# Performance work log

Measured on AMD Instinct MI355X. Metric: run time of the kernel, lower is better.

The kernel has to match this reference:

```python
import jax, jax.numpy as jnp
import numpy as np

N_HP = 49152   # healpix nodes (12 * 4**6)
N_DST = 50000  # destination feature nodes
E = 400000     # edges per edge type (avg in-degree 8)
T_OUT = 4      # output_length
H = 64         # hidden_size
HID = 128      # attention hidden = 2*hidden_size


def setup_inputs() -> dict:
    key = jax.random.key(0)
    ks = jax.random.split(key, 9)
    s = 0.1
    return {
        "x": jax.random.normal(ks[0], (N_HP, T_OUT, 1, H), jnp.float32),
        "prev0": jax.random.normal(ks[1], (N_DST, 1), jnp.float32),
        "conv_W": s * jax.random.normal(ks[2], (T_OUT, H, H), jnp.float32),
        "conv_b": jnp.zeros((T_OUT, H), jnp.float32),
        "lin_W": s * jax.random.normal(ks[3], (1, H), jnp.float32),
        "lin_b": jnp.zeros((H,), jnp.float32),
        "att_W1": s * jax.random.normal(ks[4], (H, HID), jnp.float32),
        "att_b1": jnp.zeros((HID,), jnp.float32),
        "att_W2": s * jax.random.normal(ks[5], (HID, 1), jnp.float32),
        "att_b2": jnp.zeros((1,), jnp.float32),
        "dec_W": s * jax.random.normal(ks[6], (H, 1), jnp.float32),
        "dec_b": jnp.zeros((1,), jnp.float32),
        "src_idx": jax.random.randint(ks[7], (T_OUT, E), 0, N_HP),
        "dst_idx": jax.random.randint(ks[8], (T_OUT, E), 0, N_DST),
    }


def _graph_conv(src_feat, s_idx, d_idx, W, b):
    # dgl.nn.GraphConv with norm='both', bias, activation=LeakyReLU(0.01)
    ones = jnp.ones(s_idx.shape[0], src_feat.dtype)
    out_deg = jax.ops.segment_sum(ones, s_idx, num_segments=N_HP)
    in_deg = jax.ops.segment_sum(ones, d_idx, num_segments=N_DST)
    h = src_feat * jax.lax.rsqrt(jnp.clip(out_deg, 1.0))[:, None]   # D_src^{-1/2} X
    agg = jax.ops.segment_sum(h[s_idx], d_idx, num_segments=N_DST)  # gather [E,H] + scatter-add
    agg = agg * jax.lax.rsqrt(jnp.clip(in_deg, 1.0))[:, None]       # D_dst^{-1/2}
    return jax.nn.leaky_relu(agg @ W + b, negative_slope=0.01)


def reference(x, prev0, conv_W, conv_b, lin_W, lin_b, att_W1, att_b1,
              att_W2, att_b2, dec_W, dec_b, src_idx, dst_idx):
    prev = prev0  # node data at t = input_length - 1, shape [N_DST, 1]
    outs = []
    for t in range(T_OUT):  # sequential over horizon (prev feeds back)
        feat = x[:, t, 0]  # [N_HP, H]
        # HeteroGraphConv(aggregate='sum'): every edge type's GraphConv fires
        # on the same healpix src features; per-dst-node results are summed.
        space1 = jnp.zeros((N_DST, H), x.dtype)
        for tt in range(T_OUT):
            space1 = space1 + _graph_conv(feat, src_idx[tt], dst_idx[tt],
                                          conv_W[tt], conv_b[tt])
        space2 = prev @ lin_W + lin_b            # self.linears on prev step [N_DST, H]
        s = jnp.stack([space1, space2], 0)[None]  # [1, 2, N_DST, H]
        # AttentionReadout: soft attention over dim=1 (the 2 space branches)
        logits = jnp.tanh(s @ att_W1 + att_b1) @ att_W2 + att_b2  # [1,2,N,1]
        alpha = jax.nn.softmax(logits, axis=1)
        states = (alpha * s).sum(axis=1)          # [1, N_DST, H]
        out = states @ dec_W + dec_b              # [1, N_DST, 1] (horizon=1)
        prev = out[0]                             # stored back into node data
        outs.append(prev)
    return jnp.stack(outs, axis=0)  # [T_OUT, N_DST, 1]
```

## Files before the change

kernel.cpp:

```cpp
#include <hip/hip_runtime.h>

#define N_HP 49152
#define N_DST 50000
#define NE 400000
#define H 64
#define HID 128
#define DEG_CAP 64

typedef __attribute__((ext_vector_type(8))) short bf16x8;
typedef __attribute__((ext_vector_type(4))) float f32x4;

__device__ __forceinline__ ushort f2bf(float f) {
    uint u = __float_as_uint(f);
    u += 0x7fffu + ((u >> 16) & 1);
    return (ushort)(u >> 16);
}

#define BF2LO(u) __uint_as_float((u) << 16)
#define BF2HI(u) __uint_as_float((u) & 0xffff0000u)

#define XC_N (N_HP * 64)
__global__ __launch_bounds__(256) void k_prep(const float* __restrict__ x,
                                              uint* __restrict__ xb,
                                              const int* __restrict__ src_idx,
                                              const int* __restrict__ dst_idx,
                                              int* __restrict__ cnt_src,
                                              int* __restrict__ cnt_dst,
                                              ushort* __restrict__ esrcP) {
    int tid = blockIdx.x * 256 + threadIdx.x;
    if (tid < XC_N) {
        int i = tid;
        float4 v = ((const float4*)x)[i];
        uint a = __float_as_uint(v.x), b = __float_as_uint(v.y);
        uint c = __float_as_uint(v.z), d = __float_as_uint(v.w);
        a += 0x7fffu + ((a >> 16) & 1);  b += 0x7fffu + ((b >> 16) & 1);
        c += 0x7fffu + ((c >> 16) & 1);  d += 0x7fffu + ((d >> 16) & 1);
        uint2 o;
        o.x = (a >> 16) | (b & 0xffff0000u);
        o.y = (c >> 16) | (d & 0xffff0000u);
        ((uint2*)xb)[i] = o;
    } else if (tid < XC_N + NE) {
        int i4 = tid - XC_N;
        int tt = i4 / (NE / 4);
        int4 s = ((const int4*)src_idx)[i4];
        int4 d = ((const int4*)dst_idx)[i4];
        int* cs = cnt_src + tt * N_HP;
        int* cd = cnt_dst + tt * N_DST;
        atomicAdd(&cs[s.x], 1); atomicAdd(&cs[s.y], 1);
        atomicAdd(&cs[s.z], 1); atomicAdd(&cs[s.w], 1);
        int px = atomicAdd(&cd[d.x], 1);
        int py = atomicAdd(&cd[d.y], 1);
        int pz = atomicAdd(&cd[d.z], 1);
        int pw = atomicAdd(&cd[d.w], 1);
        size_t base = (size_t)tt * N_DST * DEG_CAP;
        if (px < DEG_CAP) esrcP[base + (size_t)d.x * DEG_CAP + px] = (ushort)s.x;
        if (py < DEG_CAP) esrcP[base + (size_t)d.y * DEG_CAP + py] = (ushort)s.y;
        if (pz < DEG_CAP) esrcP[base + (size_t)d.z * DEG_CAP + pz] = (ushort)s.z;
        if (pw < DEG_CAP) esrcP[base + (size_t)d.w * DEG_CAP + pw] = (ushort)s.w;
    }
}

#define RS_N (4 * (N_HP + N_DST))
#define WP_N (4 * 4 * 2 * 64 * 8)
#define WP1_N (8 * 2 * 64 * 8)
__global__ __launch_bounds__(256) void k_small(
    const int* __restrict__ cnt_src, const int* __restrict__ cnt_dst,
    float* __restrict__ rs_out, float* __restrict__ rs_in,
    const float* __restrict__ convW, short* __restrict__ wf,
    short* __restrict__ wf1,
    const float* __restrict__ lin_W, const float* __restrict__ lin_b,
    const float* __restrict__ W1, const float* __restrict__ b1,
    const float* __restrict__ dec_W, float* __restrict__ attc) {
    int tid = blockIdx.x * 256 + threadIdx.x;
    if (tid < 4 * N_HP) {
        int c = cnt_src[tid];
        rs_out[tid] = rsqrtf((float)(c > 1 ? c : 1));
    } else if (tid < RS_N) {
        int j = tid - 4 * N_HP;
        int c = cnt_dst[j];
        rs_in[j] = rsqrtf((float)(c > 1 ? c : 1));
    } else if (tid < RS_N + WP_N) {
        int i = tid - RS_N;
        int e    = i & 7;
        int lane = (i >> 3) & 63;
        int kh   = (i >> 9) & 1;
        int tile = (i >> 10) & 3;
        int tt   = i >> 12;
        int k   = kh * 32 + (lane >> 4) * 8 + e;
        int col = tile * 16 + (lane & 15);
        wf[i] = (short)f2bf(convW[(tt * 64 + k) * 64 + col]);
    } else if (tid < RS_N + WP_N + WP1_N) {
        int i = tid - RS_N - WP_N;
        int e    = i & 7;
        int lane = (i >> 3) & 63;
        int kh   = (i >> 9) & 1;
        int jt   = i >> 10;
        int k = kh * 32 + (lane >> 4) * 8 + e;
        int j = jt * 16 + (lane & 15);
        wf1[i] = (short)f2bf(W1[k * HID + j]);
    } else if (tid < RS_N + WP_N + WP1_N + HID) {
        int j = tid - RS_N - WP_N - WP1_N;
        float c1 = 0.f, c0 = 0.f;
        for (int h = 0; h < H; ++h) {
            c1 += lin_W[h] * W1[h * HID + j];
            c0 += lin_b[h] * W1[h * HID + j];
        }
        attc[j] = c1;
        attc[HID + j] = c0 + b1[j];
    } else if (tid == RS_N + WP_N + WP1_N + HID) {
        float e1 = 0.f, e0 = 0.f;
        for (int h = 0; h < H; ++h) { e1 += lin_W[h] * dec_W[h]; e0 += lin_b[h] * dec_W[h]; }
        attc[2 * HID] = e1;
        attc[2 * HID + 1] = e0;
    }
}

__global__ __launch_bounds__(256) void k_gather(
    const uint* __restrict__ xb, const ushort* __restrict__ esrcP,
    const int* __restrict__ cnt_dst,
    const float* __restrict__ rs_out, const float* __restrict__ rs_in,
    const short* __restrict__ wf, const float* __restrict__ conv_b,
    const short* __restrict__ wf1,
    const float* __restrict__ ab1, const float* __restrict__ aW2,
    const float* __restrict__ decW,
    float* __restrict__ L0buf, float* __restrict__ P2buf) {
    const int wave = threadIdx.x >> 6, lane = threadIdx.x & 63;
    const int quad0 = (blockIdx.x * 4 + wave) * 4;
    const int t_l = lane >> 4;
    const int h0 = (lane & 15) << 2;
    const int rowA = lane & 15, grpA = lane >> 4, colA = lane & 15;
    __shared__ short A_lds[4][16 * 72];
    const uint2* x2 = (const uint2*)xb;
    const bf16x8* wf8 = (const bf16x8*)wf;
    float4 sp0 = make_float4(0.f, 0.f, 0.f, 0.f);
    float4 sp1 = make_float4(0.f, 0.f, 0.f, 0.f);
    float4 sp2 = make_float4(0.f, 0.f, 0.f, 0.f);
    float4 sp3 = make_float4(0.f, 0.f, 0.f, 0.f);

    for (int tt = 0; tt < 4; ++tt) {
        const float* rso = rs_out + tt * N_HP;
        for (int nl = 0; nl < 4; ++nl) {
            const int dst = quad0 + nl;
            int n = __builtin_amdgcn_readfirstlane(cnt_dst[tt * N_DST + dst]);
            if (n > DEG_CAP) n = DEG_CAP;
            const ushort* ep = esrcP + ((size_t)tt * N_DST + dst) * DEG_CAP;
            float4 a0 = make_float4(0.f, 0.f, 0.f, 0.f);
            float4 a1 = make_float4(0.f, 0.f, 0.f, 0.f);
            float4 a2 = make_float4(0.f, 0.f, 0.f, 0.f);
            float4 a3 = make_float4(0.f, 0.f, 0.f, 0.f);
            {
                int s0 = __builtin_amdgcn_readfirstlane((int)ep[0]);
                int s1 = __builtin_amdgcn_readfirstlane((int)ep[1]);
                int s2 = __builtin_amdgcn_readfirstlane((int)ep[2]);
                int s3 = __builtin_amdgcn_readfirstlane((int)ep[3]);
                int s4 = __builtin_amdgcn_readfirstlane((int)ep[4]);
                int s5 = __builtin_amdgcn_readfirstlane((int)ep[5]);
                int s6 = __builtin_amdgcn_readfirstlane((int)ep[6]);
                int s7 = __builtin_amdgcn_readfirstlane((int)ep[7]);
                s0 = (0 < n) ? s0 : 0;
                s1 = (1 < n) ? s1 : 0;
                s2 = (2 < n) ? s2 : 0;
                s3 = (3 < n) ? s3 : 0;
                s4 = (4 < n) ? s4 : 0;
                s5 = (5 < n) ? s5 : 0;
                s6 = (6 < n) ? s6 : 0;
                s7 = (7 < n) ? s7 : 0;
                float r0 = (0 < n) ? rso[s0] : 0.f;
                float r1 = (1 < n) ? rso[s1] : 0.f;
                float r2 = (2 < n) ? rso[s2] : 0.f;
                float r3 = (3 < n) ? rso[s3] : 0.f;
                float r4 = (4 < n) ? rso[s4] : 0.f;
                float r5 = (5 < n) ? rso[s5] : 0.f;
                float r6 = (6 < n) ? rso[s6] : 0.f;
                float r7 = (7 < n) ? rso[s7] : 0.f;
                uint2 u0 = x2[s0 * 64 + lane];
                uint2 u1 = x2[s1 * 64 + lane];
                uint2 u2 = x2[s2 * 64 + lane];
                uint2 u3 = x2[s3 * 64 + lane];
                uint2 u4 = x2[s4 * 64 + lane];
                uint2 u5 = x2[s5 * 64 + lane];
                uint2 u6 = x2[s6 * 64 + lane];
                uint2 u7 = x2[s7 * 64 + lane];
                a0.x += BF2LO(u0.x) * r0; a0.y += BF2HI(u0.x) * r0;
                a0.z += BF2LO(u0.y) * r0; a0.w += BF2HI(u0.y) * r0;
                a1.x += BF2LO(u1.x) * r1; a1.y += BF2HI(u1.x) * r1;
                a1.z += BF2LO(u1.y) * r1; a1.w += BF2HI(u1.y) * r1;
                a2.x += BF2LO(u2.x) * r2; a2.y += BF2HI(u2.x) * r2;
                a2.z += BF2LO(u2.y) * r2; a2.w += BF2HI(u2.y) * r2;
                a3.x += BF2LO(u3.x) * r3; a3.y += BF2HI(u3.x) * r3;
                a3.z += BF2LO(u3.y) * r3; a3.w += BF2HI(u3.y) * r3;
                a0.x += BF2LO(u4.x) * r4; a0.y += BF2HI(u4.x) * r4;
                a0.z += BF2LO(u4.y) * r4; a0.w += BF2HI(u4.y) * r4;
                a1.x += BF2LO(u5.x) * r5; a1.y += BF2HI(u5.x) * r5;
                a1.z += BF2LO(u5.y) * r5; a1.w += BF2HI(u5.y) * r5;
                a2.x += BF2LO(u6.x) * r6; a2.y += BF2HI(u6.x) * r6;
                a2.z += BF2LO(u6.y) * r6; a2.w += BF2HI(u6.y) * r6;
                a3.x += BF2LO(u7.x) * r7; a3.y += BF2HI(u7.x) * r7;
                a3.z += BF2LO(u7.y) * r7; a3.w += BF2HI(u7.y) * r7;
            }
            int e = 8;
            for (; e + 2 <= n; e += 2) {
                int s0 = __builtin_amdgcn_readfirstlane((int)ep[e]);
                int s1 = __builtin_amdgcn_readfirstlane((int)ep[e + 1]);
                float r0 = rso[s0], r1 = rso[s1];
                uint2 u0 = x2[s0 * 64 + lane];
                uint2 u1 = x2[s1 * 64 + lane];
                a0.x += BF2LO(u0.x) * r0; a0.y += BF2HI(u0.x) * r0;
                a0.z += BF2LO(u0.y) * r0; a0.w += BF2HI(u0.y) * r0;
                a1.x += BF2LO(u1.x) * r1; a1.y += BF2HI(u1.x) * r1;
                a1.z += BF2LO(u1.y) * r1; a1.w += BF2HI(u1.y) * r1;
            }
            if (e < n) {
                int s0 = __builtin_amdgcn_readfirstlane((int)ep[e]);
                float r0 = rso[s0];
                uint2 u0 = x2[s0 * 64 + lane];
                a0.x += BF2LO(u0.x) * r0; a0.y += BF2HI(u0.x) * r0;
                a0.z += BF2LO(u0.y) * r0; a0.w += BF2HI(u0.y) * r0;
            }
            float ri = rs_in[tt * N_DST + dst];
            float ax = (a0.x + a1.x + a2.x + a3.x) * ri;
            float ay = (a0.y + a1.y + a2.y + a3.y) * ri;
            float az = (a0.z + a1.z + a2.z + a3.z) * ri;
            float aw = (a0.w + a1.w + a2.w + a3.w) * ri;
            short4 sv;
            sv.x = (short)f2bf(ax); sv.y = (short)f2bf(ay);
            sv.z = (short)f2bf(az); sv.w = (short)f2bf(aw);
            *(short4*)&A_lds[wave][(nl * 4 + t_l) * 72 + h0] = sv;
        }
        bf16x8 af0 = *(const bf16x8*)&A_lds[wave][rowA * 72 + grpA * 8];
        bf16x8 af1 = *(const bf16x8*)&A_lds[wave][rowA * 72 + 32 + grpA * 8];
#define CONV_TILE(T, SP) { \
        bf16x8 b0 = wf8[((tt * 4 + (T)) * 2 + 0) * 64 + lane]; \
        bf16x8 b1 = wf8[((tt * 4 + (T)) * 2 + 1) * 64 + lane]; \
        f32x4 ac = {0.f, 0.f, 0.f, 0.f}; \
        ac = __builtin_amdgcn_mfma_f32_16x16x32_bf16(af0, b0, ac, 0, 0, 0); \
        ac = __builtin_amdgcn_mfma_f32_16x16x32_bf16(af1, b1, ac, 0, 0, 0); \
        float bb = conv_b[tt * 64 + (T) * 16 + colA]; \
        float m0 = ac[0] + bb, m1 = ac[1] + bb, m2 = ac[2] + bb, m3 = ac[3] + bb; \
        SP.x += m0 > 0.f ? m0 : 0.01f * m0; \
        SP.y += m1 > 0.f ? m1 : 0.01f * m1; \
        SP.z += m2 > 0.f ? m2 : 0.01f * m2; \
        SP.w += m3 > 0.f ? m3 : 0.01f * m3; }
        CONV_TILE(0, sp0)
        CONV_TILE(1, sp1)
        CONV_TILE(2, sp2)
        CONV_TILE(3, sp3)
#undef CONV_TILE
    }

#define PUT2(T, SP) { \
        A_lds[wave][(grpA * 4 + 0) * 72 + (T) * 16 + colA] = (short)f2bf(SP.x); \
        A_lds[wave][(grpA * 4 + 1) * 72 + (T) * 16 + colA] = (short)f2bf(SP.y); \
        A_lds[wave][(grpA * 4 + 2) * 72 + (T) * 16 + colA] = (short)f2bf(SP.z); \
        A_lds[wave][(grpA * 4 + 3) * 72 + (T) * 16 + colA] = (short)f2bf(SP.w); }
    PUT2(0, sp0)
    PUT2(1, sp1)
    PUT2(2, sp2)
    PUT2(3, sp3)
#undef PUT2
    float4 pp;
    {
        float dw0 = decW[0 * 16 + colA], dw1 = decW[1 * 16 + colA];
        float dw2 = decW[2 * 16 + colA], dw3 = decW[3 * 16 + colA];
        pp.x = sp0.x * dw0 + sp1.x * dw1 + sp2.x * dw2 + sp3.x * dw3;
        pp.y = sp0.y * dw0 + sp1.y * dw1 + sp2.y * dw2 + sp3.y * dw3;
        pp.z = sp0.z * dw0 + sp1.z * dw1 + sp2.z * dw2 + sp3.z * dw3;
        pp.w = sp0.w * dw0 + sp1.w * dw1 + sp2.w * dw2 + sp3.w * dw3;
    }
    bf16x8 ag0 = *(const bf16x8*)&A_lds[wave][rowA * 72 + grpA * 8];
    bf16x8 ag1 = *(const bf16x8*)&A_lds[wave][rowA * 72 + 32 + grpA * 8];
    const bf16x8* wf18 = (const bf16x8*)wf1;
    float4 la = make_float4(0.f, 0.f, 0.f, 0.f);
#pragma unroll
    for (int jt = 0; jt < 8; ++jt) {
        bf16x8 bj0 = wf18[(jt * 2 + 0) * 64 + lane];
        bf16x8 bj1 = wf18[(jt * 2 + 1) * 64 + lane];
        f32x4 c2 = {0.f, 0.f, 0.f, 0.f};
        c2 = __builtin_amdgcn_mfma_f32_16x16x32_bf16(ag0, bj0, c2, 0, 0, 0);
        c2 = __builtin_amdgcn_mfma_f32_16x16x32_bf16(ag1, bj1, c2, 0, 0, 0);
        int j = jt * 16 + colA;
        float bj = ab1[j], wj = aW2[j];
        la.x += tanhf(c2[0] + bj) * wj;
        la.y += tanhf(c2[1] + bj) * wj;
        la.z += tanhf(c2[2] + bj) * wj;
        la.w += tanhf(c2[3] + bj) * wj;
    }
    for (int off = 1; off < 16; off <<= 1) {
        la.x += __shfl_xor(la.x, off); la.y += __shfl_xor(la.y, off);
        la.z += __shfl_xor(la.z, off); la.w += __shfl_xor(la.w, off);
        pp.x += __shfl_xor(pp.x, off); pp.y += __shfl_xor(pp.y, off);
        pp.z += __shfl_xor(pp.z, off); pp.w += __shfl_xor(pp.w, off);
    }
    if (colA == 0) {
#define WOUT(R, LV, PV) { int rp = grpA * 4 + (R); \
        L0buf[(size_t)(rp & 3) * N_DST + quad0 + (rp >> 2)] = LV; \
        P2buf[(size_t)(rp & 3) * N_DST + quad0 + (rp >> 2)] = PV; }
        WOUT(0, la.x, pp.x)
        WOUT(1, la.y, pp.y)
        WOUT(2, la.z, pp.z)
        WOUT(3, la.w, pp.w)
#undef WOUT
    }
}

__global__ __launch_bounds__(512) void k_att2(
    const float* __restrict__ L0buf, const float* __restrict__ P2buf,
    const float* __restrict__ prev0,
    const float* __restrict__ W2, const float* __restrict__ b2,
    const float* __restrict__ dec_b, const float* __restrict__ attc,
    float* __restrict__ out) {
    const int wave = threadIdx.x >> 6, lane = threadIdx.x & 63;
    const int node = blockIdx.x * 8 + wave;
    const float w2a = W2[lane], w2b = W2[lane + 64];
    const float c1a = attc[lane], c1b = attc[lane + 64];
    const float c0a = attc[HID + lane], c0b = attc[HID + lane + 64];
    const float e1s = attc[2 * HID], e0s = attc[2 * HID + 1];
    const float b2s = b2[0], decb = dec_b[0];
    float prev = prev0[node];
    float l0a[4], p2a[4];
#pragma unroll
    for (int t = 0; t < 4; ++t) {
        l0a[t] = L0buf[(size_t)t * N_DST + node];
        p2a[t] = P2buf[(size_t)t * N_DST + node];
    }
#pragma unroll
    for (int t = 0; t < 4; ++t) {
        float p1 = tanhf(prev * c1a + c0a) * w2a + tanhf(prev * c1b + c0b) * w2b;
        for (int o = 32; o; o >>= 1) p1 += __shfl_xor(p1, o);
        float l0 = l0a[t] + b2s, l1 = p1 + b2s;
        float mx = fmaxf(l0, l1);
        float ea = expf(l0 - mx), eb = expf(l1 - mx);
        float inv = 1.f / (ea + eb);
        float s2d = prev * e1s + e0s;
        float ov = (ea * p2a[t] + eb * s2d) * inv + decb;
        prev = ov;
        if (lane == 0) out[(size_t)t * N_DST + node] = ov;
    }
}

extern "C" void kernel_launch(void* const* d_in, const int* in_sizes, int n_in,
                              void* d_out, int out_size, void* d_ws, size_t ws_size,
                              hipStream_t stream) {
    const float* x      = (const float*)d_in[0];
    const float* prev0  = (const float*)d_in[1];
    const float* conv_W = (const float*)d_in[2];
    const float* conv_b = (const float*)d_in[3];
    const float* lin_W  = (const float*)d_in[4];
    const float* lin_b  = (const float*)d_in[5];
    const float* att_W1 = (const float*)d_in[6];
    const float* att_b1 = (const float*)d_in[7];
    const float* att_W2 = (const float*)d_in[8];
    const float* att_b2 = (const float*)d_in[9];
    const float* dec_W  = (const float*)d_in[10];
    const float* dec_b  = (const float*)d_in[11];
    const int* src_idx  = (const int*)d_in[12];
    const int* dst_idx  = (const int*)d_in[13];
    float* out = (float*)d_out;

    char* p = (char*)d_ws;
    auto alloc = [&](size_t bytes) {
        char* q = p;
        p += (bytes + 255) & ~(size_t)255;
        return q;
    };
    int*    cnt_src = (int*)alloc((size_t)4 * N_HP * 4);
    int*    cnt_dst = (int*)alloc((size_t)4 * N_DST * 4);
    float*  rs_out  = (float*)alloc((size_t)4 * N_HP * 4);
    float*  rs_in   = (float*)alloc((size_t)4 * N_DST * 4);
    ushort* esrcP   = (ushort*)alloc((size_t)4 * N_DST * DEG_CAP * 2);
    float*  attc    = (float*)alloc((size_t)(2 * HID + 2) * 4);
    short*  wf      = (short*)alloc((size_t)4 * 64 * 64 * 2);
    short*  wf1     = (short*)alloc((size_t)64 * 128 * 2);
    float*  L0buf   = (float*)alloc((size_t)4 * N_DST * 4);
    float*  P2buf   = (float*)alloc((size_t)4 * N_DST * 4);
    uint*   xbf     = (uint*)alloc((size_t)N_HP * 256 * 2);

    hipMemsetAsync(cnt_src, 0, (size_t)((char*)rs_out - (char*)cnt_src), stream);

    k_prep<<<(XC_N + NE + 255) / 256, 256, 0, stream>>>(x, xbf, src_idx, dst_idx,
                                                        cnt_src, cnt_dst, esrcP);
    k_small<<<(RS_N + WP_N + WP1_N + HID + 1 + 255) / 256, 256, 0, stream>>>(
        cnt_src, cnt_dst, rs_out, rs_in, conv_W, wf, wf1,
        lin_W, lin_b, att_W1, att_b1, dec_W, attc);
    k_gather<<<N_DST / 16, 256, 0, stream>>>(xbf, esrcP, cnt_dst, rs_out, rs_in,
                                             wf, conv_b, wf1, att_b1, att_W2, dec_W,
                                             L0buf, P2buf);
    k_att2<<<N_DST / 8, 512, 0, stream>>>(L0buf, P2buf, prev0,
                                          att_W2, att_b2, dec_b, attc, out);
}
```

Before: 348.8 us.

## Fuse attention recurrence into gather kernel and compute in-degree norm inline

Moves the sequential attention-readout recurrence from a separate k_att2 kernel into the tail of k_gather. Each dst node's 128-wide tanh projection is split across 16 lanes with 8 elements each and reduced with xor shuffles. The in-degree rsqrt is now computed inline from the count already loaded, instead of being precomputed into rs_in. This removes one launch and the L0/P2 intermediate buffer round trip, at the cost of extra per-lane tanh work and register pressure in the gather kernel.

Result: faster. 323.0 us (-7.4%).

```diff
diff --git a/kernel.cpp b/kernel.cpp
--- a/kernel.cpp
+++ b/kernel.cpp
@@ -60,27 +60,23 @@
     }
 }
 
-#define RS_N (4 * (N_HP + N_DST))
+#define RS2_N (4 * N_HP)
 #define WP_N (4 * 4 * 2 * 64 * 8)
 #define WP1_N (8 * 2 * 64 * 8)
 __global__ __launch_bounds__(256) void k_small(
-    const int* __restrict__ cnt_src, const int* __restrict__ cnt_dst,
-    float* __restrict__ rs_out, float* __restrict__ rs_in,
+    const int* __restrict__ cnt_src,
+    float* __restrict__ rs_out,
     const float* __restrict__ convW, short* __restrict__ wf,
     short* __restrict__ wf1,
     const float* __restrict__ lin_W, const float* __restrict__ lin_b,
     const float* __restrict__ W1, const float* __restrict__ b1,
     const float* __restrict__ dec_W, float* __restrict__ attc) {
     int tid = blockIdx.x * 256 + threadIdx.x;
-    if (tid < 4 * N_HP) {
+    if (tid < RS2_N) {
         int c = cnt_src[tid];
         rs_out[tid] = rsqrtf((float)(c > 1 ? c : 1));
-    } else if (tid < RS_N) {
-        int j = tid - 4 * N_HP;
-        int c = cnt_dst[j];
-        rs_in[j] = rsqrtf((float)(c > 1 ? c : 1));
-    } else if (tid < RS_N + WP_N) {
-        int i = tid - RS_N;
+    } else if (tid < RS2_N + WP_N) {
+        int i = tid - RS2_N;
         int e    = i & 7;
         int lane = (i >> 3) & 63;
         int kh   = (i >> 9) & 1;
@@ -89,8 +85,8 @@
         int k   = kh * 32 + (lane >> 4) * 8 + e;
         int col = tile * 16 + (lane & 15);
         wf[i] = (short)f2bf(convW[(tt * 64 + k) * 64 + col]);
-    } else if (tid < RS_N + WP_N + WP1_N) {
-        int i = tid - RS_N - WP_N;
+    } else if (tid < RS2_N + WP_N + WP1_N) {
+        int i = tid - RS2_N - WP_N;
         int e    = i & 7;
         int lane = (i >> 3) & 63;
         int kh   = (i >> 9) & 1;
@@ -98,8 +94,8 @@
         int k = kh * 32 + (lane >> 4) * 8 + e;
         int j = jt * 16 + (lane & 15);
         wf1[i] = (short)f2bf(W1[k * HID + j]);
-    } else if (tid < RS_N + WP_N + WP1_N + HID) {
-        int j = tid - RS_N - WP_N - WP1_N;
+    } else if (tid < RS2_N + WP_N + WP1_N + HID) {
+        int j = tid - RS2_N - WP_N - WP1_N;
         float c1 = 0.f, c0 = 0.f;
         for (int h = 0; h < H; ++h) {
             c1 += lin_W[h] * W1[h * HID + j];
@@ -107,7 +103,7 @@
         }
         attc[j] = c1;
         attc[HID + j] = c0 + b1[j];
-    } else if (tid == RS_N + WP_N + WP1_N + HID) {
+    } else if (tid == RS2_N + WP_N + WP1_N + HID) {
         float e1 = 0.f, e0 = 0.f;
         for (int h = 0; h < H; ++h) { e1 += lin_W[h] * dec_W[h]; e0 += lin_b[h] * dec_W[h]; }
         attc[2 * HID] = e1;
@@ -118,12 +114,14 @@
 __global__ __launch_bounds__(256) void k_gather(
     const uint* __restrict__ xb, const ushort* __restrict__ esrcP,
     const int* __restrict__ cnt_dst,
-    const float* __restrict__ rs_out, const float* __restrict__ rs_in,
+    const float* __restrict__ rs_out,
     const short* __restrict__ wf, const float* __restrict__ conv_b,
     const short* __restrict__ wf1,
     const float* __restrict__ ab1, const float* __restrict__ aW2,
     const float* __restrict__ decW,
-    float* __restrict__ L0buf, float* __restrict__ P2buf) {
+    const float* __restrict__ prev0, const float* __restrict__ attc,
+    const float* __restrict__ b2, const float* __restrict__ dec_b,
+    float* __restrict__ out) {
     const int wave = threadIdx.x >> 6, lane = threadIdx.x & 63;
     const int quad0 = (blockIdx.x * 4 + wave) * 4;
     const int t_l = lane >> 4;
@@ -141,8 +139,8 @@
         const float* rso = rs_out + tt * N_HP;
         for (int nl = 0; nl < 4; ++nl) {
             const int dst = quad0 + nl;
-            int n = __builtin_amdgcn_readfirstlane(cnt_dst[tt * N_DST + dst]);
-            if (n > DEG_CAP) n = DEG_CAP;
+            int n_raw = __builtin_amdgcn_readfirstlane(cnt_dst[tt * N_DST + dst]);
+            int n = n_raw > DEG_CAP ? DEG_CAP : n_raw;
             const ushort* ep = esrcP + ((size_t)tt * N_DST + dst) * DEG_CAP;
             float4 a0 = make_float4(0.f, 0.f, 0.f, 0.f);
             float4 a1 = make_float4(0.f, 0.f, 0.f, 0.f);
@@ -217,7 +215,7 @@
                 a0.x += BF2LO(u0.x) * r0; a0.y += BF2HI(u0.x) * r0;
                 a0.z += BF2LO(u0.y) * r0; a0.w += BF2HI(u0.y) * r0;
             }
-            float ri = rs_in[tt * N_DST + dst];
+            float ri = rsqrtf((float)(n_raw > 1 ? n_raw : 1));
             float ax = (a0.x + a1.x + a2.x + a3.x) * ri;
             float ay = (a0.y + a1.y + a2.y + a3.y) * ri;
             float az = (a0.z + a1.z + a2.z + a3.z) * ri;
@@ -291,51 +289,38 @@
         pp.x += __shfl_xor(pp.x, off); pp.y += __shfl_xor(pp.y, off);
         pp.z += __shfl_xor(pp.z, off); pp.w += __shfl_xor(pp.w, off);
     }
-    if (colA == 0) {
-#define WOUT(R, LV, PV) { int rp = grpA * 4 + (R); \
-        L0buf[(size_t)(rp & 3) * N_DST + quad0 + (rp >> 2)] = LV; \
-        P2buf[(size_t)(rp & 3) * N_DST + quad0 + (rp >> 2)] = PV; }
-        WOUT(0, la.x, pp.x)
-        WOUT(1, la.y, pp.y)
-        WOUT(2, la.z, pp.z)
-        WOUT(3, la.w, pp.w)
-#undef WOUT
-    }
-}
-
-__global__ __launch_bounds__(512) void k_att2(
-    const float* __restrict__ L0buf, const float* __restrict__ P2buf,
-    const float* __restrict__ prev0,
-    const float* __restrict__ W2, const float* __restrict__ b2,
-    const float* __restrict__ dec_b, const float* __restrict__ attc,
-    float* __restrict__ out) {
-    const int wave = threadIdx.x >> 6, lane = threadIdx.x & 63;
-    const int node = blockIdx.x * 8 + wave;
-    const float w2a = W2[lane], w2b = W2[lane + 64];
-    const float c1a = attc[lane], c1b = attc[lane + 64];
-    const float c0a = attc[HID + lane], c0b = attc[HID + lane + 64];
+
+    float c1j[8], c0j[8], w2j[8];
+#pragma unroll
+    for (int i = 0; i < 8; ++i) {
+        int j = colA * 8 + i;
+        c1j[i] = attc[j];
+        c0j[i] = attc[HID + j];
+        w2j[i] = aW2[j];
+    }
     const float e1s = attc[2 * HID], e0s = attc[2 * HID + 1];
     const float b2s = b2[0], decb = dec_b[0];
+    const int node = quad0 + grpA;
     float prev = prev0[node];
-    float l0a[4], p2a[4];
-#pragma unroll
-    for (int t = 0; t < 4; ++t) {
-        l0a[t] = L0buf[(size_t)t * N_DST + node];
-        p2a[t] = P2buf[(size_t)t * N_DST + node];
-    }
-#pragma unroll
-    for (int t = 0; t < 4; ++t) {
-        float p1 = tanhf(prev * c1a + c0a) * w2a + tanhf(prev * c1b + c0b) * w2b;
-        for (int o = 32; o; o >>= 1) p1 += __shfl_xor(p1, o);
-        float l0 = l0a[t] + b2s, l1 = p1 + b2s;
-        float mx = fmaxf(l0, l1);
-        float ea = expf(l0 - mx), eb = expf(l1 - mx);
-        float inv = 1.f / (ea + eb);
-        float s2d = prev * e1s + e0s;
-        float ov = (ea * p2a[t] + eb * s2d) * inv + decb;
-        prev = ov;
-        if (lane == 0) out[(size_t)t * N_DST + node] = ov;
-    }
+#define CHAIN(LV, PV, T) { \
+    float p1 = 0.f; \
+    _Pragma("unroll") \
+    for (int i = 0; i < 8; ++i) p1 += tanhf(prev * c1j[i] + c0j[i]) * w2j[i]; \
+    p1 += __shfl_xor(p1, 1); p1 += __shfl_xor(p1, 2); \
+    p1 += __shfl_xor(p1, 4); p1 += __shfl_xor(p1, 8); \
+    float l0 = (LV) + b2s, l1 = p1 + b2s; \
+    float mx = fmaxf(l0, l1); \
+    float ea = expf(l0 - mx), eb = expf(l1 - mx); \
+    float inv = 1.f / (ea + eb); \
+    float s2d = prev * e1s + e0s; \
+    float ov = (ea * (PV) + eb * s2d) * inv + decb; \
+    prev = ov; \
+    if (colA == 0) out[(size_t)(T) * N_DST + node] = ov; }
+    CHAIN(la.x, pp.x, 0)
+    CHAIN(la.y, pp.y, 1)
+    CHAIN(la.z, pp.z, 2)
+    CHAIN(la.w, pp.w, 3)
+#undef CHAIN
 }
 
 extern "C" void kernel_launch(void* const* d_in, const int* in_sizes, int n_in,
@@ -366,25 +351,20 @@
     int*    cnt_src = (int*)alloc((size_t)4 * N_HP * 4);
     int*    cnt_dst = (int*)alloc((size_t)4 * N_DST * 4);
     float*  rs_out  = (float*)alloc((size_t)4 * N_HP * 4);
-    float*  rs_in   = (float*)alloc((size_t)4 * N_DST * 4);
     ushort* esrcP   = (ushort*)alloc((size_t)4 * N_DST * DEG_CAP * 2);
     float*  attc    = (float*)alloc((size_t)(2 * HID + 2) * 4);
     short*  wf      = (short*)alloc((size_t)4 * 64 * 64 * 2);
     short*  wf1     = (short*)alloc((size_t)64 * 128 * 2);
-    float*  L0buf   = (float*)alloc((size_t)4 * N_DST * 4);
-    float*  P2buf   = (float*)alloc((size_t)4 * N_DST * 4);
     uint*   xbf     = (uint*)alloc((size_t)N_HP * 256 * 2);
 
     hipMemsetAsync(cnt_src, 0, (size_t)((char*)rs_out - (char*)cnt_src), stream);
 
     k_prep<<<(XC_N + NE + 255) / 256, 256, 0, stream>>>(x, xbf, src_idx, dst_idx,
                                                         cnt_src, cnt_dst, esrcP);
-    k_small<<<(RS_N + WP_N + WP1_N + HID + 1 + 255) / 256, 256, 0, stream>>>(
-        cnt_src, cnt_dst, rs_out, rs_in, conv_W, wf, wf1,
+    k_small<<<(RS2_N + WP_N + WP1_N + HID + 1 + 255) / 256, 256, 0, stream>>>(
+        cnt_src, rs_out, conv_W, wf, wf1,
         lin_W, lin_b, att_W1, att_b1, dec_W, attc);
-    k_gather<<<N_DST / 16, 256, 0, stream>>>(xbf, esrcP, cnt_dst, rs_out, rs_in,
+    k_gather<<<N_DST / 16, 256, 0, stream>>>(xbf, esrcP, cnt_dst, rs_out,
                                              wf, conv_b, wf1, att_b1, att_W2, dec_W,
-                                             L0buf, P2buf);
-    k_att2<<<N_DST / 8, 512, 0, stream>>>(L0buf, P2buf, prev0,
-                                          att_W2, att_b2, dec_b, attc, out);
-}
+                                             prev0, attc, att_b2, dec_b, out);
+}
```
